# Performance work log

Measured on AMD Instinct MI355X. Metric: run time of the kernel, lower is better.

Reference implementation:

```python
import jax, jax.numpy as jnp
import numpy as np
import math

D_MODEL = 1024
D_STATE = 128
EXPAND = 2
HEADDIM = 64
NGROUPS = 1
ROPE_FRACTION = 0.5
A_FLOOR = 1e-4
D_INNER = EXPAND * D_MODEL            # 2048
NHEADS = D_INNER // HEADDIM           # 32
SPLIT = int(D_STATE * ROPE_FRACTION)  # 64
R = SPLIT // 2                        # 32 rotary angles; rotary applied to first R state dims
D_IN_PROJ = 2 * D_INNER + 2 * D_STATE * NGROUPS + 3 * NHEADS + R  # 4480
BATCH = 1
SEQLEN = 1024


def setup_inputs() -> dict:
    key = jax.random.key(0)
    k0, k1, k2, k3 = jax.random.split(key, 4)
    u = jax.random.normal(k0, (BATCH, SEQLEN, D_MODEL), jnp.float32)
    w_in = jax.random.normal(k1, (D_IN_PROJ, D_MODEL), jnp.float32) * (D_MODEL ** -0.5)
    w_out = jax.random.normal(k2, (D_MODEL, D_INNER), jnp.float32) * (D_INNER ** -0.5)
    # dt_bias init matches torch: inverse-softplus of dt ~ LogUniform(dt_min, dt_max)
    dt = jnp.exp(jax.random.uniform(k3, (NHEADS,), jnp.float32)
                 * (math.log(0.1) - math.log(0.001)) + math.log(0.001))
    dt = jnp.maximum(dt, 1e-4)
    dt_bias = dt + jnp.log(-jnp.expm1(-dt))
    D = jnp.ones((NHEADS,), jnp.float32)
    return {"u": u, "w_in": w_in, "w_out": w_out, "dt_bias": dt_bias, "D": D}


def _mamba3_forward(u, w_in, w_out, dt_bias, D):
    b, l, _ = u.shape
    proj = u @ w_in.T  # [b, l, D_IN_PROJ]
    sizes = [D_INNER, D_INNER, D_STATE * NGROUPS, D_STATE * NGROUPS, NHEADS, NHEADS, NHEADS, R]
    idx = np.cumsum(sizes)[:-1]
    z, x, B, C, dd_dt, dd_A, trap, angles = jnp.split(proj, idx, axis=-1)

    A = jnp.minimum(-jax.nn.softplus(dd_A), -A_FLOOR)      # [b,l,h]
    dt = jax.nn.softplus(dd_dt + dt_bias)                  # [b,l,h]
    tr = jax.nn.sigmoid(trap)                              # [b,l,h]
    # rotary angle: tanh(angles)[b,l,1,R] * dt[b,l,h,1] * pi, cumsum over time
    theta = jnp.cumsum(jnp.tanh(angles)[:, :, None, :] * dt[..., None] * jnp.pi, axis=1)  # [b,l,h,R]

    x_h = x.reshape(b, l, NHEADS, HEADDIM)
    z_h = z.reshape(b, l, NHEADS, HEADDIM)
    B_h = B.reshape(b, l, NGROUPS, D_STATE)[:, :, 0, :]  # only group 0 is read in the loop
    C_h = C.reshape(b, l, NGROUPS, D_STATE)[:, :, 0, :]

    def step(carry, inp):
        sr, si, px = carry  # sr: [b,h,p,n], si: [b,h,p,R] (imag beyond R is identically zero)
        dt_t, A_t, tr_t, th, bt, ct, xt = inp
        alpha = jnp.exp(A_t * dt_t)[:, :, None, None]          # [b,h,1,1]
        beta = ((1.0 - tr_t) * dt_t)[:, :, None, None] * alpha
        gamma = (tr_t * dt_t)[:, :, None, None]
        base = bt[:, None, None, :] * (px[..., None] * beta + xt[..., None] * gamma)  # [b,h,p,n]
        rc = jnp.cos(th)[:, :, None, :]  # [b,h,1,R]
        rs = jnp.sin(th)[:, :, None, :]
        sr = sr * alpha + jnp.concatenate([base[..., :R] * rc, base[..., R:]], axis=-1)
        si = si * alpha + base[..., :R] * rs
        ctb = ct[:, None, None, :]
        y = (jnp.sum((sr[..., :R] * rc + si * rs) * ctb[..., :R], axis=-1)
             + jnp.sum(sr[..., R:] * ctb[..., R:], axis=-1))  # [b,h,p]
        return (sr, si, xt), y

    sr0 = jnp.zeros((b, NHEADS, HEADDIM, D_STATE), u.dtype)
    si0 = jnp.zeros((b, NHEADS, HEADDIM, R), u.dtype)
    px0 = jnp.zeros((b, NHEADS, HEADDIM), u.dtype)
    xs = (jnp.moveaxis(dt, 1, 0), jnp.moveaxis(A, 1, 0), jnp.moveaxis(tr, 1, 0),
          jnp.moveaxis(theta, 1, 0), jnp.moveaxis(B_h, 1, 0), jnp.moveaxis(C_h, 1, 0),
          jnp.moveaxis(x_h, 1, 0))
    _, ys = jax.lax.scan(step, (sr0, si0, px0), xs)  # [l,b,h,p]
    y = jnp.moveaxis(ys, 0, 1) + D[None, None, :, None] * x_h
    out = y * jax.nn.silu(z_h)
    return out.reshape(b, l, D_INNER) @ w_out.T


def reference(u, w_in, w_out, dt_bias, D):
    return _mamba3_forward(u, w_in, w_out, dt_bias, D)
```

## Files before the change

kernel.cpp:

```cpp
#include <hip/hip_runtime.h>
#include <math.h>

#define L_SEQ   1024
#define DMODEL  1024
#define DINNER  2048
#define NH      32
#define HD      64
#define NS      160
#define RR      32
#define NPROJ   4480
#define OFF_Z   0
#define OFF_X   2048
#define OFF_B   4096
#define OFF_C   4224
#define OFF_DT  4352
#define OFF_A   4384
#define OFF_TR  4416
#define OFF_ANG 4448
#define NC      16
#define CL      64
#define PIF     3.14159265358979323846f

typedef __attribute__((ext_vector_type(8))) short bf16x8;
typedef __attribute__((ext_vector_type(4))) float f32x4;
typedef unsigned int u32;
typedef unsigned short u16;

__device__ __forceinline__ float softplusf(float x) {
  return (x > 20.f) ? x : log1pf(expf(x));
}
__device__ __forceinline__ u16 f2bf(float f) {
  u32 u = __float_as_uint(f);
  u32 r = (u + 0x7FFFu + ((u >> 16) & 1u)) >> 16;
  return (u16)r;
}
__device__ __forceinline__ float bf2f(u16 v) {
  return __uint_as_float(((u32)v) << 16);
}

__device__ __forceinline__ void gload_lds16(const u16* g, u16* l) {
  __builtin_amdgcn_global_load_lds(
      (const __attribute__((address_space(1))) u32*)(unsigned long long)(const void*)g,
      (__attribute__((address_space(3))) u32*)(unsigned long long)(void*)l, 16, 0, 0);
}

__global__ __launch_bounds__(256) void cvt_bf16(
    const float* __restrict__ src, u16* __restrict__ dst, int n8) {
  int i = blockIdx.x * 256 + threadIdx.x;
  if (i >= n8) return;
  const float4* s4 = (const float4*)src;
  float4 a = s4[2 * i], b = s4[2 * i + 1];
  union { u16 h[8]; uint4 v; } o;
  o.h[0] = f2bf(a.x); o.h[1] = f2bf(a.y); o.h[2] = f2bf(a.z); o.h[3] = f2bf(a.w);
  o.h[4] = f2bf(b.x); o.h[5] = f2bf(b.y); o.h[6] = f2bf(b.z); o.h[7] = f2bf(b.w);
  ((uint4*)dst)[i] = o.v;
}

template <int BM, int BN>
__global__ __launch_bounds__(256) void gemm_bf16(
    const u16* __restrict__ A, const u16* __restrict__ B,
    float* __restrict__ C, int N, int K) {
  constexpr int BK = 32;
  constexpr int WM = BM / 2, WN = BN / 2;
  constexpr int MF = WM / 16, NF = WN / 16;
  constexpr int CA = BM / 64;
  constexpr int CB = BN / 64;
  __shared__ u16 lds[(BM + BN) * BK];

  const int bm = blockIdx.y * BM, bn = blockIdx.x * BN;
  const int tid = threadIdx.x, w = tid >> 6, lane = tid & 63;
  const int wr = w >> 1, wc = w & 1;
  const int fr = lane & 15, sl = lane >> 4;
  const int lrow = lane >> 2, lslot = (lane & 3) * 8;

  const u16* gA[CA]; u16* lA[CA];
#pragma unroll
  for (int j = 0; j < CA; ++j) {
    int ca = w * CA + j;
    gA[j] = A + (size_t)(bm + ca * 16 + lrow) * K + lslot;
    lA[j] = lds + ca * 512;
  }
  const u16* gB[CB]; u16* lB[CB];
#pragma unroll
  for (int j = 0; j < CB; ++j) {
    int cb = w * CB + j;
    gB[j] = B + (size_t)(bn + cb * 16 + lrow) * K + lslot;
    lB[j] = lds + BM * 32 + cb * 512;
  }

  const u16* aptr[MF]; const u16* bptr[NF];
#pragma unroll
  for (int i = 0; i < MF; ++i)
    aptr[i] = lds + (wr * WM + i * 16 + fr) * 32 + sl * 8;
#pragma unroll
  for (int j = 0; j < NF; ++j)
    bptr[j] = lds + BM * 32 + (wc * WN + j * 16 + fr) * 32 + sl * 8;

  f32x4 acc[MF][NF] = {};
  const int iters = K / BK;

#pragma unroll
  for (int j = 0; j < CA; ++j) gload_lds16(gA[j], lA[j]);
#pragma unroll
  for (int j = 0; j < CB; ++j) gload_lds16(gB[j], lB[j]);

  for (int it = 0; it < iters; ++it) {
    __syncthreads();
    bf16x8 af[MF], bfv[NF];
#pragma unroll
    for (int i = 0; i < MF; ++i) af[i] = *(const bf16x8*)aptr[i];
#pragma unroll
    for (int j = 0; j < NF; ++j) bfv[j] = *(const bf16x8*)bptr[j];
    __syncthreads();
    if (it + 1 < iters) {
#pragma unroll
      for (int j = 0; j < CA; ++j) gload_lds16(gA[j] + (it + 1) * BK, lA[j]);
#pragma unroll
      for (int j = 0; j < CB; ++j) gload_lds16(gB[j] + (it + 1) * BK, lB[j]);
    }
#pragma unroll
    for (int i = 0; i < MF; ++i)
#pragma unroll
      for (int j = 0; j < NF; ++j)
        acc[i][j] = __builtin_amdgcn_mfma_f32_16x16x32_bf16(
            af[i], bfv[j], acc[i][j], 0, 0, 0);
  }

#pragma unroll
  for (int i = 0; i < MF; ++i) {
    int rb = bm + wr * WM + i * 16 + sl * 4;
#pragma unroll
    for (int j = 0; j < NF; ++j) {
      int cb = bn + wc * WN + j * 16 + fr;
#pragma unroll
      for (int r = 0; r < 4; ++r)
        C[(size_t)(rb + r) * N + cb] = acc[i][j][r];
    }
  }
}

__global__ __launch_bounds__(256) void prep_scalars(
    const float* __restrict__ proj, const float* __restrict__ dt_bias,
    float* __restrict__ dtA, float* __restrict__ lnaA,
    float* __restrict__ betaA, float* __restrict__ gammaA,
    float* __restrict__ angP) {
  int idx = blockIdx.x * 256 + threadIdx.x;
  int h = idx & 31, l = idx >> 5;
  const float* prow = proj + (size_t)l * NPROJ;
  float dt = softplusf(prow[OFF_DT + h] + dt_bias[h]);
  float Apos = fmaxf(softplusf(prow[OFF_A + h]), 1e-4f);
  float tr = 1.f / (1.f + expf(-prow[OFF_TR + h]));
  float lna = -Apos * dt;
  float alpha = expf(lna);
  dtA[idx] = dt;
  lnaA[idx] = lna;
  betaA[idx] = (1.f - tr) * dt * alpha;
  gammaA[idx] = tr * dt;
  angP[idx] = tanhf(prow[OFF_ANG + h]) * PIF;
}

__global__ __launch_bounds__(256) void theta_scan(
    const float* __restrict__ angP, const float* __restrict__ dtA,
    float* __restrict__ rc, float* __restrict__ rs) {
  const int h = blockIdx.x >> 5;
  const int r = blockIdx.x & 31;
  const int tid = threadIdx.x;
  __shared__ float ldssc[256];

  float csum[4];
  float run = 0.f;
#pragma unroll
  for (int i = 0; i < 4; ++i) {
    int l = tid * 4 + i;
    run += angP[l * NH + r] * dtA[l * NH + h];
    csum[i] = run;
  }
  ldssc[tid] = run;
  __syncthreads();
  for (int off = 1; off < 256; off <<= 1) {
    float t = (tid >= off) ? ldssc[tid - off] : 0.f;
    __syncthreads();
    ldssc[tid] += t;
    __syncthreads();
  }
  float excl = ldssc[tid] - run;
#pragma unroll
  for (int i = 0; i < 4; ++i) {
    int l = tid * 4 + i;
    float th = excl + csum[i];
    size_t o = ((size_t)l * NH + h) * RR + r;
    rc[o] = cosf(th);
    rs[o] = sinf(th);
  }
}

__global__ __launch_bounds__(256) void prep_uvg(
    const float* __restrict__ proj, const float* __restrict__ betaA,
    const float* __restrict__ gammaA, const float* __restrict__ lnaA,
    const float* __restrict__ rc, const float* __restrict__ rs,
    u16* __restrict__ U, u16* __restrict__ V, u16* __restrict__ Gt,
    float* __restrict__ cumA, float* __restrict__ adec) {
  const int h = blockIdx.x >> 4, c = blockIdx.x & 15;
  const int c0 = c * CL;
  const int tid = threadIdx.x;
  const int w = tid >> 6, lane = tid & 63;
  __shared__ float xs[65][64];
  __shared__ float bet[64], gam[64];

  for (int i = tid; i < 65 * 16; i += 256) {
    int r = i >> 4, c4 = i & 15;
    int l = c0 - 1 + r;
    float4 v = {0.f, 0.f, 0.f, 0.f};
    if (l >= 0)
      v = *(const float4*)(proj + (size_t)l * NPROJ + OFF_X + h * HD + c4 * 4);
    *(float4*)&xs[r][c4 * 4] = v;
  }
  if (tid < 64) {
    bet[tid] = betaA[(c0 + tid) * NH + h];
    gam[tid] = gammaA[(c0 + tid) * NH + h];
  }
  __syncthreads();

  {
    const int p = lane;
    union { u16 hh[16]; uint4 q[2]; } o;
    float xprev = xs[w * 16][p];
#pragma unroll
    for (int i = 0; i < 16; ++i) {
      int s = w * 16 + i;
      float xcur = xs[s + 1][p];
      o.hh[i] = f2bf(bet[s] * xprev + gam[s] * xcur);
      xprev = xcur;
    }
    uint4* dst = (uint4*)(Gt + (((size_t)h * NC + c) * HD + p) * CL + w * 16);
    dst[0] = o.q[0];
    dst[1] = o.q[1];
  }

  if (tid < 160) {
    const int n = tid;
    const int idxB = (n < 64) ? (n & 31) : (n - 32);
    const bool is_re = (n < 32);
    const bool has_rot = (n < 64);
    for (int ss = 0; ss < 64; ++ss) {
      int l = c0 + ss;
      const float* prow = proj + (size_t)l * NPROJ;
      float Bv = prow[OFF_B + idxB];
      float Cv = prow[OFF_C + idxB];
      if (has_rot) {
        float rv = is_re ? rc[((size_t)l * NH + h) * RR + idxB]
                         : rs[((size_t)l * NH + h) * RR + idxB];
        Bv *= rv;
        Cv *= rv;
      }
      U[((size_t)h * L_SEQ + l) * NS + n] = f2bf(Cv);
      V[((size_t)h * L_SEQ + l) * NS + n] = f2bf(Bv);
    }
  } else if (tid >= 192) {
    const int t = tid - 192;
    float v = lnaA[(c0 + t) * NH + h];
#pragma unroll
    for (int k = 1; k < 64; k <<= 1) {
      int src = t - k;
      float o = __shfl(v, src < 0 ? 0 : src);
      if (t >= k) v += o;
    }
    cumA[(size_t)h * L_SEQ + c0 + t] = v;
    if (t == 63) adec[h * NC + c] = expf(v);
  }
}

__global__ __launch_bounds__(256) void passA(
    const u16* __restrict__ V, const u16* __restrict__ Gt,
    const float* __restrict__ cumA, float* __restrict__ S) {
  const int c = blockIdx.x >> 5, h = blockIdx.x & 31;
  const int c0 = c * CL;
  const int tid = threadIdx.x;
  const int w = tid >> 6, lane = tid & 63;
  const int wr = w >> 1, wc = w & 1;
  const int fr = lane & 15, sl = lane >> 4;
  __shared__ u16 Vl[64][168];
  __shared__ u16 Vt[160][72];
  __shared__ u16 Gw[64][72];
  __shared__ float wsc[64];

  const u16* Vsrc = V + ((size_t)h * L_SEQ + c0) * NS;
  for (int i = tid; i < 64 * 20; i += 256) {
    int r = i / 20, ch = i % 20;
    *(uint4*)&Vl[r][ch * 8] = *(const uint4*)(Vsrc + (size_t)r * NS + ch * 8);
  }
  if (tid < 64) {
    float last = cumA[(size_t)h * L_SEQ + c0 + 63];
    wsc[tid] = expf(last - cumA[(size_t)h * L_SEQ + c0 + tid]);
  }
  __syncthreads();

  if (tid < 160) {
    int n = tid;
#pragma unroll
    for (int s2 = 0; s2 < 32; ++s2) {
      u32 lo = Vl[2 * s2][n], hi = Vl[2 * s2 + 1][n];
      *(u32*)&Vt[n][2 * s2] = lo | (hi << 16);
    }
  }
  {
    const u16* Gsrc = Gt + ((size_t)h * NC + c) * HD * CL;
    for (int i = tid; i < 64 * 8; i += 256) {
      int p = i >> 3, ch = i & 7;
      uint4 raw = *(const uint4*)(Gsrc + (size_t)p * CL + ch * 8);
      u16* rh = (u16*)&raw;
      union { u16 hh[8]; uint4 q; } o;
#pragma unroll
      for (int j = 0; j < 8; ++j)
        o.hh[j] = f2bf(bf2f(rh[j]) * wsc[ch * 8 + j]);
      *(uint4*)&Gw[p][ch * 8] = o.q;
    }
  }
  __syncthreads();

  f32x4 acc[2][5] = {};
#pragma unroll
  for (int ks = 0; ks < 2; ++ks) {
    bf16x8 a0 = *(const bf16x8*)&Gw[wr * 32 + fr][ks * 32 + sl * 8];
    bf16x8 a1 = *(const bf16x8*)&Gw[wr * 32 + 16 + fr][ks * 32 + sl * 8];
    bf16x8 bv[5];
#pragma unroll
    for (int fj = 0; fj < 5; ++fj)
      bv[fj] = *(const bf16x8*)&Vt[wc * 80 + fj * 16 + fr][ks * 32 + sl * 8];
#pragma unroll
    for (int fj = 0; fj < 5; ++fj) {
      acc[0][fj] = __builtin_amdgcn_mfma_f32_16x16x32_bf16(a0, bv[fj], acc[0][fj], 0, 0, 0);
      acc[1][fj] = __builtin_amdgcn_mfma_f32_16x16x32_bf16(a1, bv[fj], acc[1][fj], 0, 0, 0);
    }
  }
  float* Fb = S + (size_t)(c * NH + h) * HD * NS;
#pragma unroll
  for (int fi = 0; fi < 2; ++fi)
#pragma unroll
    for (int fj = 0; fj < 5; ++fj)
#pragma unroll
      for (int r = 0; r < 4; ++r) {
        int p = wr * 32 + fi * 16 + sl * 4 + r;
        int n = wc * 80 + fj * 16 + fr;
        Fb[(size_t)p * NS + n] = acc[fi][fj][r];
      }
}

__global__ __launch_bounds__(256) void combine(
    float* __restrict__ S, const float* __restrict__ adec) {
  const int idx = blockIdx.x * 256 + threadIdx.x;
  if (idx >= NH * HD * NS) return;
  const int n = idx % NS;
  const int rem = idx / NS;
  const int p = rem & 63;
  const int h = rem >> 6;
  float F = 0.f;
  for (int c = 0; c < NC; ++c) {
    size_t off = ((size_t)(c * NH + h) * HD + p) * NS + n;
    float sv = S[off];
    S[off] = F;
    F = fmaf(F, adec[h * NC + c], sv);
  }
}

__global__ __launch_bounds__(256) void passB(
    const float* __restrict__ proj, const u16* __restrict__ U,
    const u16* __restrict__ V, const u16* __restrict__ Gt,
    const float* __restrict__ cumA, const float* __restrict__ S,
    const float* __restrict__ Dvec, u16* __restrict__ yz) {
  const int c = blockIdx.x >> 5, h = blockIdx.x & 31;
  const int c0 = c * CL;
  const int tid = threadIdx.x;
  const int w = tid >> 6, lane = tid & 63;
  const int wr = w >> 1, wc = w & 1;
  const int fr = lane & 15, sl = lane >> 4;
  __shared__ u16 Ul[64][168];
  __shared__ u16 BB[64][168];
  __shared__ u16 Ml[64][72];
  __shared__ u16 Gl[64][72];
  __shared__ float cums[64], ecum[64];

  const u16* Us = U + ((size_t)h * L_SEQ + c0) * NS;
  for (int i = tid; i < 1280; i += 256) {
    int r = i / 20, ch = i % 20;
    *(uint4*)&Ul[r][ch * 8] = *(const uint4*)(Us + (size_t)r * NS + ch * 8);
  }
  {
    const float* S0 = S + (size_t)(c * NH + h) * HD * NS;
    int r = tid >> 2, q4 = tid & 3;
#pragma unroll
    for (int i = 0; i < 10; ++i) {
      int ch = q4 * 10 + i;
      float4 f = *(const float4*)(S0 + (size_t)r * NS + ch * 4);
      u32 lo = (u32)f2bf(f.x) | ((u32)f2bf(f.y) << 16);
      u32 hi = (u32)f2bf(f.z) | ((u32)f2bf(f.w) << 16);
      *(u32*)&BB[r][ch * 4] = lo;
      *(u32*)&BB[r][ch * 4 + 2] = hi;
    }
  }
  if (tid < 64) {
    float cv = cumA[(size_t)h * L_SEQ + c0 + tid];
    cums[tid] = cv;
    ecum[tid] = expf(cv);
  }
  __syncthreads();

  f32x4 acc[2][2] = {};
#pragma unroll
  for (int ks = 0; ks < 5; ++ks) {
    bf16x8 a0 = *(const bf16x8*)&Ul[wr * 32 + fr][ks * 32 + sl * 8];
    bf16x8 a1 = *(const bf16x8*)&Ul[wr * 32 + 16 + fr][ks * 32 + sl * 8];
    bf16x8 b0 = *(const bf16x8*)&BB[wc * 32 + fr][ks * 32 + sl * 8];
    bf16x8 b1 = *(const bf16x8*)&BB[wc * 32 + 16 + fr][ks * 32 + sl * 8];
    acc[0][0] = __builtin_amdgcn_mfma_f32_16x16x32_bf16(a0, b0, acc[0][0], 0, 0, 0);
    acc[0][1] = __builtin_amdgcn_mfma_f32_16x16x32_bf16(a0, b1, acc[0][1], 0, 0, 0);
    acc[1][0] = __builtin_amdgcn_mfma_f32_16x16x32_bf16(a1, b0, acc[1][0], 0, 0, 0);
    acc[1][1] = __builtin_amdgcn_mfma_f32_16x16x32_bf16(a1, b1, acc[1][1], 0, 0, 0);
  }
#pragma unroll
  for (int fi = 0; fi < 2; ++fi)
#pragma unroll
    for (int fj = 0; fj < 2; ++fj)
#pragma unroll
      for (int r = 0; r < 4; ++r)
        acc[fi][fj][r] *= ecum[wr * 32 + fi * 16 + sl * 4 + r];
  __syncthreads();

  const u16* Vs = V + ((size_t)h * L_SEQ + c0) * NS;
  for (int i = tid; i < 1280; i += 256) {
    int r = i / 20, ch = i % 20;
    *(uint4*)&BB[r][ch * 8] = *(const uint4*)(Vs + (size_t)r * NS + ch * 8);
  }
  const u16* Gs = Gt + ((size_t)h * NC + c) * HD * CL;
  for (int i = tid; i < 512; i += 256) {
    int p = i >> 3, ch = i & 7;
    *(uint4*)&Gl[p][ch * 8] = *(const uint4*)(Gs + (size_t)p * CL + ch * 8);
  }
  __syncthreads();

  f32x4 pac[2][2] = {};
#pragma unroll
  for (int ks = 0; ks < 5; ++ks) {
    bf16x8 a0 = *(const bf16x8*)&Ul[wr * 32 + fr][ks * 32 + sl * 8];
    bf16x8 a1 = *(const bf16x8*)&Ul[wr * 32 + 16 + fr][ks * 32 + sl * 8];
    bf16x8 b0 = *(const bf16x8*)&BB[wc * 32 + fr][ks * 32 + sl * 8];
    bf16x8 b1 = *(const bf16x8*)&BB[wc * 32 + 16 + fr][ks * 32 + sl * 8];
    pac[0][0] = __builtin_amdgcn_mfma_f32_16x16x32_bf16(a0, b0, pac[0][0], 0, 0, 0);
    pac[0][1] = __builtin_amdgcn_mfma_f32_16x16x32_bf16(a0, b1, pac[0][1], 0, 0, 0);
    pac[1][0] = __builtin_amdgcn_mfma_f32_16x16x32_bf16(a1, b0, pac[1][0], 0, 0, 0);
    pac[1][1] = __builtin_amdgcn_mfma_f32_16x16x32_bf16(a1, b1, pac[1][1], 0, 0, 0);
  }
#pragma unroll
  for (int fi = 0; fi < 2; ++fi)
#pragma unroll
    for (int fj = 0; fj < 2; ++fj)
#pragma unroll
      for (int r = 0; r < 4; ++r) {
        int t = wr * 32 + fi * 16 + sl * 4 + r;
        int ss = wc * 32 + fj * 16 + fr;
        float m = (ss <= t) ? expf(cums[t] - cums[ss]) * pac[fi][fj][r] : 0.f;
        Ml[t][ss] = f2bf(m);
      }
  __syncthreads();

#pragma unroll
  for (int ks = 0; ks < 2; ++ks) {
    bf16x8 a0 = *(const bf16x8*)&Ml[wr * 32 + fr][ks * 32 + sl * 8];
    bf16x8 a1 = *(const bf16x8*)&Ml[wr * 32 + 16 + fr][ks * 32 + sl * 8];
    bf16x8 b0 = *(const bf16x8*)&Gl[wc * 32 + fr][ks * 32 + sl * 8];
    bf16x8 b1 = *(const bf16x8*)&Gl[wc * 32 + 16 + fr][ks * 32 + sl * 8];
    acc[0][0] = __builtin_amdgcn_mfma_f32_16x16x32_bf16(a0, b0, acc[0][0], 0, 0, 0);
    acc[0][1] = __builtin_amdgcn_mfma_f32_16x16x32_bf16(a0, b1, acc[0][1], 0, 0, 0);
    acc[1][0] = __builtin_amdgcn_mfma_f32_16x16x32_bf16(a1, b0, acc[1][0], 0, 0, 0);
    acc[1][1] = __builtin_amdgcn_mfma_f32_16x16x32_bf16(a1, b1, acc[1][1], 0, 0, 0);
  }

  const float Dh = Dvec[h];
#pragma unroll
  for (int fi = 0; fi < 2; ++fi)
#pragma unroll
    for (int fj = 0; fj < 2; ++fj)
#pragma unroll
      for (int r = 0; r < 4; ++r) {
        int t = wr * 32 + fi * 16 + sl * 4 + r;
        int p = wc * 32 + fj * 16 + fr;
        int l = c0 + t;
        float x = proj[(size_t)l * NPROJ + OFF_X + h * HD + p];
        float z = proj[(size_t)l * NPROJ + OFF_Z + h * HD + p];
        float y = acc[fi][fj][r] + Dh * x;
        float sg = z / (1.f + expf(-z));
        yz[(size_t)l * DINNER + h * HD + p] = f2bf(y * sg);
      }
}

extern "C" void kernel_launch(void* const* d_in, const int* in_sizes, int n_in,
                              void* d_out, int out_size, void* d_ws, size_t ws_size,
                              hipStream_t stream) {
  const float* u       = (const float*)d_in[0];
  const float* w_in    = (const float*)d_in[1];
  const float* w_out   = (const float*)d_in[2];
  const float* dt_bias = (const float*)d_in[3];
  const float* Dvec    = (const float*)d_in[4];
  float* out = (float*)d_out;

  float* ws = (float*)d_ws;
  float* proj   = ws;
  float* dtA    = proj + 4587520;
  float* lnaA   = dtA + 32768;
  float* betaA  = lnaA + 32768;
  float* gammaA = betaA + 32768;
  float* cumA   = gammaA + 32768;
  float* adec   = cumA + 32768;
  float* angP   = adec + 512;
  float* Sbuf   = angP + 32768;
  u16*   Gtb    = (u16*)(Sbuf + 5242880);
  u16*   Ubuf   = Gtb + 2097152;
  u16*   Vbuf   = Ubuf + 5242880;
  u16*   yzb    = Vbuf + 5242880;
  u16*   ub   = (u16*)Sbuf;
  u16*   wib  = ub + 1048576;
  float* rcb  = Sbuf;
  float* rsb  = rcb + 1048576;
  u16*   wob  = (u16*)Sbuf;

  cvt_bf16<<<(1048576 / 8 + 255) / 256, 256, 0, stream>>>(u, ub, 1048576 / 8);
  cvt_bf16<<<(4587520 / 8 + 255) / 256, 256, 0, stream>>>(w_in, wib, 4587520 / 8);

  gemm_bf16<128, 128><<<dim3(NPROJ / 128, L_SEQ / 128), 256, 0, stream>>>(
      ub, wib, proj, NPROJ, DMODEL);

  prep_scalars<<<(L_SEQ * NH) / 256, 256, 0, stream>>>(
      proj, dt_bias, dtA, lnaA, betaA, gammaA, angP);

  theta_scan<<<NH * RR, 256, 0, stream>>>(angP, dtA, rcb, rsb);

  prep_uvg<<<NH * NC, 256, 0, stream>>>(
      proj, betaA, gammaA, lnaA, rcb, rsb, Ubuf, Vbuf, Gtb, cumA, adec);

  passA<<<NC * NH, 256, 0, stream>>>(Vbuf, Gtb, cumA, Sbuf);

  combine<<<(NH * HD * NS + 255) / 256, 256, 0, stream>>>(Sbuf, adec);

  passB<<<NC * NH, 256, 0, stream>>>(
      proj, Ubuf, Vbuf, Gtb, cumA, Sbuf, Dvec, yzb);

  cvt_bf16<<<(2097152 / 8 + 255) / 256, 256, 0, stream>>>(w_out, wob, 2097152 / 8);

  gemm_bf16<64, 64><<<dim3(DMODEL / 64, L_SEQ / 64), 256, 0, stream>>>(
      yzb, wob, out, DMODEL, DINNER);
}
```

Before: 150.7 us.

## Fuse conversions and passA into neighbors, store chunk states in bf16

Merges the u and w_in conversions into one launch and folds the w_out conversion into the scalar-prep kernel. The separate passA state-computation kernel is fused into the U/V/G prep kernel, which keeps V and the decay-weighted G in shared memory instead of reloading them. Chunk states are now stored in bf16 rather than fp32, halving their traffic through combine and passB. The result is fewer launches, but the combine recurrence now reads and writes rounded bf16 values, which costs some accuracy.

```diff
diff --git a/kernel.cpp b/kernel.cpp
--- a/kernel.cpp
+++ b/kernel.cpp
@@ -44,16 +44,19 @@
       (__attribute__((address_space(3))) u32*)(unsigned long long)(void*)l, 16, 0, 0);
 }
 
-__global__ __launch_bounds__(256) void cvt_bf16(
-    const float* __restrict__ src, u16* __restrict__ dst, int n8) {
+__global__ __launch_bounds__(256) void cvt2_bf16(
+    const float* __restrict__ s0, u16* __restrict__ d0, int q0,
+    const float* __restrict__ s1, u16* __restrict__ d1, int q1) {
   int i = blockIdx.x * 256 + threadIdx.x;
-  if (i >= n8) return;
-  const float4* s4 = (const float4*)src;
-  float4 a = s4[2 * i], b = s4[2 * i + 1];
+  const float* s; u16* d; int j;
+  if (i < q0) { s = s0; d = d0; j = i; }
+  else { j = i - q0; if (j >= q1) return; s = s1; d = d1; }
+  const float4* s4 = (const float4*)s;
+  float4 a = s4[2 * j], b = s4[2 * j + 1];
   union { u16 h[8]; uint4 v; } o;
   o.h[0] = f2bf(a.x); o.h[1] = f2bf(a.y); o.h[2] = f2bf(a.z); o.h[3] = f2bf(a.w);
   o.h[4] = f2bf(b.x); o.h[5] = f2bf(b.y); o.h[6] = f2bf(b.z); o.h[7] = f2bf(b.w);
-  ((uint4*)dst)[i] = o.v;
+  ((uint4*)d)[j] = o.v;
 }
 
 template <int BM, int BN>
@@ -139,12 +142,24 @@
   }
 }
 
-__global__ __launch_bounds__(256) void prep_scalars(
+__global__ __launch_bounds__(256) void prep_scalars_cvt(
     const float* __restrict__ proj, const float* __restrict__ dt_bias,
     float* __restrict__ dtA, float* __restrict__ lnaA,
     float* __restrict__ betaA, float* __restrict__ gammaA,
-    float* __restrict__ angP) {
-  int idx = blockIdx.x * 256 + threadIdx.x;
+    float* __restrict__ angP,
+    const float* __restrict__ wsrc, u16* __restrict__ wdst) {
+  const int b = blockIdx.x;
+  if (b < 1024) {
+    int j = b * 256 + threadIdx.x;
+    const float4* s4 = (const float4*)wsrc;
+    float4 a = s4[2 * j], bb = s4[2 * j + 1];
+    union { u16 h[8]; uint4 v; } o;
+    o.h[0] = f2bf(a.x); o.h[1] = f2bf(a.y); o.h[2] = f2bf(a.z); o.h[3] = f2bf(a.w);
+    o.h[4] = f2bf(bb.x); o.h[5] = f2bf(bb.y); o.h[6] = f2bf(bb.z); o.h[7] = f2bf(bb.w);
+    ((uint4*)wdst)[j] = o.v;
+    return;
+  }
+  int idx = (b - 1024) * 256 + threadIdx.x;
   int h = idx & 31, l = idx >> 5;
   const float* prow = proj + (size_t)l * NPROJ;
   float dt = softplusf(prow[OFF_DT + h] + dt_bias[h]);
@@ -194,48 +209,74 @@
   }
 }
 
-__global__ __launch_bounds__(256) void prep_uvg(
+__global__ __launch_bounds__(256) void uvgA(
     const float* __restrict__ proj, const float* __restrict__ betaA,
     const float* __restrict__ gammaA, const float* __restrict__ lnaA,
     const float* __restrict__ rc, const float* __restrict__ rs,
     u16* __restrict__ U, u16* __restrict__ V, u16* __restrict__ Gt,
-    float* __restrict__ cumA, float* __restrict__ adec) {
+    float* __restrict__ cumA, float* __restrict__ adec,
+    u16* __restrict__ S) {
   const int h = blockIdx.x >> 4, c = blockIdx.x & 15;
   const int c0 = c * CL;
   const int tid = threadIdx.x;
   const int w = tid >> 6, lane = tid & 63;
-  __shared__ float xs[65][64];
-  __shared__ float bet[64], gam[64];
-
-  for (int i = tid; i < 65 * 16; i += 256) {
-    int r = i >> 4, c4 = i & 15;
-    int l = c0 - 1 + r;
-    float4 v = {0.f, 0.f, 0.f, 0.f};
-    if (l >= 0)
-      v = *(const float4*)(proj + (size_t)l * NPROJ + OFF_X + h * HD + c4 * 4);
-    *(float4*)&xs[r][c4 * 4] = v;
-  }
-  if (tid < 64) {
-    bet[tid] = betaA[(c0 + tid) * NH + h];
-    gam[tid] = gammaA[(c0 + tid) * NH + h];
+
+  __shared__ __attribute__((aligned(16))) char smem[54784];
+  u16 (*Gw)[72]   = (u16(*)[72])(smem);
+  float* wsc      = (float*)(smem + 9216);
+  float* bet      = (float*)(smem + 9472);
+  float* gam      = (float*)(smem + 9728);
+  float (*xs)[64] = (float(*)[64])(smem + 10240);
+  u16 (*Vl)[168]  = (u16(*)[168])(smem + 10240);
+  u16 (*Vt)[72]   = (u16(*)[72])(smem + 31744);
+
+  if (w < 3) {
+    for (int i = tid; i < 65 * 16; i += 192) {
+      int r = i >> 4, c4 = i & 15;
+      int l = c0 - 1 + r;
+      float4 v = {0.f, 0.f, 0.f, 0.f};
+      if (l >= 0)
+        v = *(const float4*)(proj + (size_t)l * NPROJ + OFF_X + h * HD + c4 * 4);
+      *(float4*)&xs[r][c4 * 4] = v;
+    }
+  } else {
+    const int t = lane;
+    float v = lnaA[(c0 + t) * NH + h];
+#pragma unroll
+    for (int k = 1; k < 64; k <<= 1) {
+      int src = t - k;
+      float o = __shfl(v, src < 0 ? 0 : src);
+      if (t >= k) v += o;
+    }
+    cumA[(size_t)h * L_SEQ + c0 + t] = v;
+    if (t == 63) adec[h * NC + c] = expf(v);
+    float c63 = __shfl(v, 63);
+    wsc[t] = expf(c63 - v);
+    bet[t] = betaA[(c0 + t) * NH + h];
+    gam[t] = gammaA[(c0 + t) * NH + h];
   }
   __syncthreads();
 
   {
     const int p = lane;
-    union { u16 hh[16]; uint4 q[2]; } o;
+    union { u16 hh[16]; uint4 q[2]; } og, ow;
     float xprev = xs[w * 16][p];
 #pragma unroll
     for (int i = 0; i < 16; ++i) {
       int s = w * 16 + i;
       float xcur = xs[s + 1][p];
-      o.hh[i] = f2bf(bet[s] * xprev + gam[s] * xcur);
+      float g = bet[s] * xprev + gam[s] * xcur;
+      og.hh[i] = f2bf(g);
+      ow.hh[i] = f2bf(g * wsc[s]);
       xprev = xcur;
     }
-    uint4* dst = (uint4*)(Gt + (((size_t)h * NC + c) * HD + p) * CL + w * 16);
-    dst[0] = o.q[0];
-    dst[1] = o.q[1];
-  }
+    uint4* gdst = (uint4*)(Gt + (((size_t)h * NC + c) * HD + p) * CL + w * 16);
+    gdst[0] = og.q[0];
+    gdst[1] = og.q[1];
+    *(uint4*)&Gw[p][w * 16] = ow.q[0];
+    *(uint4*)&Gw[p][w * 16 + 8] = ow.q[1];
+  }
+  __syncthreads();
 
   if (tid < 160) {
     const int n = tid;
@@ -250,48 +291,13 @@
       if (has_rot) {
         float rv = is_re ? rc[((size_t)l * NH + h) * RR + idxB]
                          : rs[((size_t)l * NH + h) * RR + idxB];
-        Bv *= rv;
-        Cv *= rv;
+        Bv *= rv; Cv *= rv;
       }
+      u16 bb = f2bf(Bv);
       U[((size_t)h * L_SEQ + l) * NS + n] = f2bf(Cv);
-      V[((size_t)h * L_SEQ + l) * NS + n] = f2bf(Bv);
-    }
-  } else if (tid >= 192) {
-    const int t = tid - 192;
-    float v = lnaA[(c0 + t) * NH + h];
-#pragma unroll
-    for (int k = 1; k < 64; k <<= 1) {
-      int src = t - k;
-      float o = __shfl(v, src < 0 ? 0 : src);
-      if (t >= k) v += o;
-    }
-    cumA[(size_t)h * L_SEQ + c0 + t] = v;
-    if (t == 63) adec[h * NC + c] = expf(v);
-  }
-}
-
-__global__ __launch_bounds__(256) void passA(
-    const u16* __restrict__ V, const u16* __restrict__ Gt,
-    const float* __restrict__ cumA, float* __restrict__ S) {
-  const int c = blockIdx.x >> 5, h = blockIdx.x & 31;
-  const int c0 = c * CL;
-  const int tid = threadIdx.x;
-  const int w = tid >> 6, lane = tid & 63;
-  const int wr = w >> 1, wc = w & 1;
-  const int fr = lane & 15, sl = lane >> 4;
-  __shared__ u16 Vl[64][168];
-  __shared__ u16 Vt[160][72];
-  __shared__ u16 Gw[64][72];
-  __shared__ float wsc[64];
-
-  const u16* Vsrc = V + ((size_t)h * L_SEQ + c0) * NS;
-  for (int i = tid; i < 64 * 20; i += 256) {
-    int r = i / 20, ch = i % 20;
-    *(uint4*)&Vl[r][ch * 8] = *(const uint4*)(Vsrc + (size_t)r * NS + ch * 8);
-  }
-  if (tid < 64) {
-    float last = cumA[(size_t)h * L_SEQ + c0 + 63];
-    wsc[tid] = expf(last - cumA[(size_t)h * L_SEQ + c0 + tid]);
+      V[((size_t)h * L_SEQ + l) * NS + n] = bb;
+      Vl[ss][n] = bb;
+    }
   }
   __syncthreads();
 
@@ -303,21 +309,10 @@
       *(u32*)&Vt[n][2 * s2] = lo | (hi << 16);
     }
   }
-  {
-    const u16* Gsrc = Gt + ((size_t)h * NC + c) * HD * CL;
-    for (int i = tid; i < 64 * 8; i += 256) {
-      int p = i >> 3, ch = i & 7;
-      uint4 raw = *(const uint4*)(Gsrc + (size_t)p * CL + ch * 8);
-      u16* rh = (u16*)&raw;
-      union { u16 hh[8]; uint4 q; } o;
-#pragma unroll
-      for (int j = 0; j < 8; ++j)
-        o.hh[j] = f2bf(bf2f(rh[j]) * wsc[ch * 8 + j]);
-      *(uint4*)&Gw[p][ch * 8] = o.q;
-    }
-  }
-  __syncthreads();
-
+  __syncthreads();
+
+  const int wr = w >> 1, wc = w & 1;
+  const int fr = lane & 15, sl = lane >> 4;
   f32x4 acc[2][5] = {};
 #pragma unroll
   for (int ks = 0; ks < 2; ++ks) {
@@ -333,7 +328,7 @@
       acc[1][fj] = __builtin_amdgcn_mfma_f32_16x16x32_bf16(a1, bv[fj], acc[1][fj], 0, 0, 0);
     }
   }
-  float* Fb = S + (size_t)(c * NH + h) * HD * NS;
+  u16* Fb = S + (size_t)(c * NH + h) * HD * NS;
 #pragma unroll
   for (int fi = 0; fi < 2; ++fi)
 #pragma unroll
@@ -342,12 +337,12 @@
       for (int r = 0; r < 4; ++r) {
         int p = wr * 32 + fi * 16 + sl * 4 + r;
         int n = wc * 80 + fj * 16 + fr;
-        Fb[(size_t)p * NS + n] = acc[fi][fj][r];
+        Fb[(size_t)p * NS + n] = f2bf(acc[fi][fj][r]);
       }
 }
 
 __global__ __launch_bounds__(256) void combine(
-    float* __restrict__ S, const float* __restrict__ adec) {
+    u16* __restrict__ S, const float* __restrict__ adec) {
   const int idx = blockIdx.x * 256 + threadIdx.x;
   if (idx >= NH * HD * NS) return;
   const int n = idx % NS;
@@ -357,8 +352,8 @@
   float F = 0.f;
   for (int c = 0; c < NC; ++c) {
     size_t off = ((size_t)(c * NH + h) * HD + p) * NS + n;
-    float sv = S[off];
-    S[off] = F;
+    float sv = bf2f(S[off]);
+    S[off] = f2bf(F);
     F = fmaf(F, adec[h * NC + c], sv);
   }
 }
@@ -366,7 +361,7 @@
 __global__ __launch_bounds__(256) void passB(
     const float* __restrict__ proj, const u16* __restrict__ U,
     const u16* __restrict__ V, const u16* __restrict__ Gt,
-    const float* __restrict__ cumA, const float* __restrict__ S,
+    const float* __restrict__ cumA, const u16* __restrict__ S,
     const float* __restrict__ Dvec, u16* __restrict__ yz) {
   const int c = blockIdx.x >> 5, h = blockIdx.x & 31;
   const int c0 = c * CL;
@@ -386,16 +381,10 @@
     *(uint4*)&Ul[r][ch * 8] = *(const uint4*)(Us + (size_t)r * NS + ch * 8);
   }
   {
-    const float* S0 = S + (size_t)(c * NH + h) * HD * NS;
-    int r = tid >> 2, q4 = tid & 3;
-#pragma unroll
-    for (int i = 0; i < 10; ++i) {
-      int ch = q4 * 10 + i;
-      float4 f = *(const float4*)(S0 + (size_t)r * NS + ch * 4);
-      u32 lo = (u32)f2bf(f.x) | ((u32)f2bf(f.y) << 16);
-      u32 hi = (u32)f2bf(f.z) | ((u32)f2bf(f.w) << 16);
-      *(u32*)&BB[r][ch * 4] = lo;
-      *(u32*)&BB[r][ch * 4 + 2] = hi;
+    const u16* S0 = S + (size_t)(c * NH + h) * HD * NS;
+    for (int i = tid; i < 1280; i += 256) {
+      int r = i / 20, ch = i % 20;
+      *(uint4*)&BB[r][ch * 8] = *(const uint4*)(S0 + (size_t)r * NS + ch * 8);
     }
   }
   if (tid < 64) {
@@ -512,39 +501,35 @@
   float* cumA   = gammaA + 32768;
   float* adec   = cumA + 32768;
   float* angP   = adec + 512;
-  float* Sbuf   = angP + 32768;
-  u16*   Gtb    = (u16*)(Sbuf + 5242880);
+  float* rcb    = angP + 32768;
+  float* rsb    = rcb + 1048576;
+  u16*   Sb     = (u16*)(rsb + 1048576);
+  u16*   Gtb    = Sb + 5242880;
   u16*   Ubuf   = Gtb + 2097152;
   u16*   Vbuf   = Ubuf + 5242880;
   u16*   yzb    = Vbuf + 5242880;
-  u16*   ub   = (u16*)Sbuf;
-  u16*   wib  = ub + 1048576;
-  float* rcb  = Sbuf;
-  float* rsb  = rcb + 1048576;
-  u16*   wob  = (u16*)Sbuf;
-
-  cvt_bf16<<<(1048576 / 8 + 255) / 256, 256, 0, stream>>>(u, ub, 1048576 / 8);
-  cvt_bf16<<<(4587520 / 8 + 255) / 256, 256, 0, stream>>>(w_in, wib, 4587520 / 8);
+  u16*   wob    = yzb + 2097152;
+  u16*   ub     = Ubuf;
+  u16*   wib    = Ubuf + 1048576;
+
+  cvt2_bf16<<<(131072 + 573440) / 256, 256, 0, stream>>>(
+      u, ub, 131072, w_in, wib, 573440);
 
   gemm_bf16<128, 128><<<dim3(NPROJ / 128, L_SEQ / 128), 256, 0, stream>>>(
       ub, wib, proj, NPROJ, DMODEL);
 
-  prep_scalars<<<(L_SEQ * NH) / 256, 256, 0, stream>>>(
-      proj, dt_bias, dtA, lnaA, betaA, gammaA, angP);
+  prep_scalars_cvt<<<1024 + 128, 256, 0, stream>>>(
+      proj, dt_bias, dtA, lnaA, betaA, gammaA, angP, w_out, wob);
 
   theta_scan<<<NH * RR, 256, 0, stream>>>(angP, dtA, rcb, rsb);
 
-  prep_uvg<<<NH * NC, 256, 0, stream>>>(
-      proj, betaA, gammaA, lnaA, rcb, rsb, Ubuf, Vbuf, Gtb, cumA, adec);
-
-  passA<<<NC * NH, 256, 0, stream>>>(Vbuf, Gtb, cumA, Sbuf);
-
-  combine<<<(NH * HD * NS + 255) / 256, 256, 0, stream>>>(Sbuf, adec);
+  uvgA<<<NH * NC, 256, 0, stream>>>(
+      proj, betaA, gammaA, lnaA, rcb, rsb, Ubuf, Vbuf, Gtb, cumA, adec, Sb);
+
+  combine<<<(NH * HD * NS + 255) / 256, 256, 0, stream>>>(Sb, adec);
 
   passB<<<NC * NH, 256, 0, stream>>>(
-      proj, Ubuf, Vbuf, Gtb, cumA, Sbuf, Dvec, yzb);
-
-  cvt_bf16<<<(2097152 / 8 + 255) / 256, 256, 0, stream>>>(w_out, wob, 2097152 / 8);
+      proj, Ubuf, Vbuf, Gtb, cumA, Sb, Dvec, yzb);
 
   gemm_bf16<64, 64><<<dim3(DMODEL / 64, L_SEQ / 64), 256, 0, stream>>>(
       yzb, wob, out, DMODEL, DINNER);
```

Measured after the change: 133.9 us. 1.12x faster.
